# Kernel optimization log

Hardware: AMD Instinct MI355X
Metric: run time of the kernel (lower is better)

## Reference

```python
import jax, jax.numpy as jnp
import numpy as np

B, N, D, DH = 8, 2048, 1024, 64

def setup_inputs() -> dict:
    key = jax.random.key(0)
    ks = jax.random.split(key, 4)
    s = 1.0 / np.sqrt(D)
    return {
        "x": jax.random.normal(ks[0], (B, N, D), dtype=jnp.float32),
        "Wq": jax.random.normal(ks[1], (D, DH), dtype=jnp.float32) * s,
        "bq": jnp.zeros((DH,), dtype=jnp.float32),
        "Wk": jax.random.normal(ks[2], (D, DH), dtype=jnp.float32) * s,
        "bk": jnp.zeros((DH,), dtype=jnp.float32),
        "Wv": jax.random.normal(ks[3], (D, DH), dtype=jnp.float32) * s,
        "bv": jnp.zeros((DH,), dtype=jnp.float32),
    }

def reference(x, Wq, bq, Wk, bk, Wv, bv):
    # Projections: [B,N,DH]
    Q = x @ Wq + bq
    K = x @ Wk + bk
    V = x @ Wv + bv
    sqrt_dh = jnp.sqrt(jnp.asarray(DH, dtype=x.dtype))
    # scores[b,i,j] = Q_i . K_j  (original materializes [B,N,N,DH]; GEMM is equivalent math)
    att = jnp.einsum("bid,bjd->bij", Q, K) / sqrt_dh
    # NOTE: original softmaxes over dim=1 (the query/i axis), not the usual j axis.
    att = jax.nn.softmax(att, axis=1)
    # Dropout is identity in eval mode.
    return jnp.einsum("bij,bjd->bid", att, V)
```

## Files before the change

### kernel.cpp

```cpp
#include <hip/hip_runtime.h>
#include <math.h>

#define Bn  8
#define Nn  2048
#define Dn  1024
#define DHn 64
#define PAD  72
#define PADP 72

typedef __attribute__((ext_vector_type(8))) short bf16x8;
typedef __attribute__((ext_vector_type(4))) float f32x4;

static __device__ inline short f2bf(float f) {
    unsigned u = __builtin_bit_cast(unsigned, f);
    u += 0x7FFFu + ((u >> 16) & 1u);
    return (short)(u >> 16);
}
static __device__ inline bf16x8 pack8(float4 a, float4 b) {
    bf16x8 v;
    v[0] = f2bf(a.x); v[1] = f2bf(a.y); v[2] = f2bf(a.z); v[3] = f2bf(a.w);
    v[4] = f2bf(b.x); v[5] = f2bf(b.y); v[6] = f2bf(b.z); v[7] = f2bf(b.w);
    return v;
}

__global__ __launch_bounds__(128) void wt_kernel(
    const float* __restrict__ Wq, const float* __restrict__ Wk,
    const float* __restrict__ Wv, short* __restrict__ Wtf)
{
    const int nt = blockIdx.x / 16, kt = blockIdx.x % 16;
    const int t = threadIdx.x;
    const int half = t >> 6, l = t & 63;
    const int c = l & 15, quad = l >> 4;
    const int mat = nt >> 2, cm = (nt & 3) * 16 + c;
    const float* Wm = (mat == 0) ? Wq : (mat == 1 ? Wk : Wv);
    short* o = &Wtf[((((size_t)nt * 16 + kt) * 2 + half) * 64 + l) * 8];
#pragma unroll
    for (int e = 0; e < 8; ++e) {
        const int k = kt * 64 + half * 32 + quad * 8 + e;
        o[e] = f2bf(Wm[(size_t)k * DHn + cm]);
    }
}

__global__ __launch_bounds__(256) void qkv_kernel(
    const float* __restrict__ x, const short* __restrict__ Wtf,
    const float* __restrict__ bq, const float* __restrict__ bk,
    const float* __restrict__ bv,
    short* __restrict__ Qb, short* __restrict__ Kb, short* __restrict__ Vt)
{
    __shared__ __attribute__((aligned(16))) short xs[2][32][PAD];

    const int t = threadIdx.x;
    const int w = t >> 6, l = t & 63;
    const int c = l & 15, quad = l >> 4;
    const int ibase = blockIdx.x * 32;
    const int r0 = t >> 3, kc = t & 7;

    const float* xrow = &x[(size_t)(ibase + r0) * Dn + kc * 8];

    {
        const float4 a = ((const float4*)xrow)[0];
        const float4 b = ((const float4*)xrow)[1];
        *(bf16x8*)&xs[0][r0][kc * 8] = pack8(a, b);
    }

    f32x4 acc[2][3];
#pragma unroll
    for (int mt = 0; mt < 2; ++mt)
#pragma unroll
        for (int nt = 0; nt < 3; ++nt) acc[mt][nt] = (f32x4){0.f, 0.f, 0.f, 0.f};

    __syncthreads();

    for (int kt = 0; kt < 16; ++kt) {
        const int cur = kt & 1;
        float4 pa, pb;
        if (kt < 15) {
            pa = ((const float4*)(xrow + (kt + 1) * 64))[0];
            pb = ((const float4*)(xrow + (kt + 1) * 64))[1];
        }
#pragma unroll
        for (int h = 0; h < 2; ++h) {
            const bf16x8 af0 = *(const bf16x8*)&xs[cur][c][h * 32 + quad * 8];
            const bf16x8 af1 = *(const bf16x8*)&xs[cur][16 + c][h * 32 + quad * 8];
#pragma unroll
            for (int nt = 0; nt < 3; ++nt) {
                const int ntg = w * 3 + nt;
                const bf16x8 bf = *(const bf16x8*)&Wtf[((((size_t)ntg * 16 + kt) * 2 + h) * 64 + l) * 8];
                acc[0][nt] = __builtin_amdgcn_mfma_f32_16x16x32_bf16(af0, bf, acc[0][nt], 0, 0, 0);
                acc[1][nt] = __builtin_amdgcn_mfma_f32_16x16x32_bf16(af1, bf, acc[1][nt], 0, 0, 0);
            }
        }
        if (kt < 15) *(bf16x8*)&xs[1 - cur][r0][kc * 8] = pack8(pa, pb);
        __syncthreads();
    }

#pragma unroll
    for (int nt = 0; nt < 3; ++nt) {
        const int col = w * 48 + nt * 16 + c;
        const int mat = col >> 6, cm = col & 63;
        const float bias = (mat == 0 ? bq : (mat == 1 ? bk : bv))[cm];
#pragma unroll
        for (int mt = 0; mt < 2; ++mt) {
            if (mat == 2) {
                const int row = ibase + mt * 16 + quad * 4;
                const int b = row >> 11, i = row & (Nn - 1);
                ushort4 o;
                o.x = (unsigned short)f2bf(acc[mt][nt][0] + bias);
                o.y = (unsigned short)f2bf(acc[mt][nt][1] + bias);
                o.z = (unsigned short)f2bf(acc[mt][nt][2] + bias);
                o.w = (unsigned short)f2bf(acc[mt][nt][3] + bias);
                *(ushort4*)&Vt[((size_t)b * DHn + cm) * Nn + i] = o;
            } else {
                const float s = (mat == 1) ? 0.125f : 1.0f;
                short* Out = (mat == 0) ? Qb : Kb;
#pragma unroll
                for (int r = 0; r < 4; ++r)
                    Out[(size_t)(ibase + mt * 16 + quad * 4 + r) * DHn + cm] =
                        f2bf((acc[mt][nt][r] + bias) * s);
            }
        }
    }
}

__global__ __launch_bounds__(256) void colsum_kernel(
    const short* __restrict__ Qb, const short* __restrict__ Kb,
    float* __restrict__ lpart)
{
    __shared__ __attribute__((aligned(16))) short Qw[4][2][32][PAD];
    __shared__ float red[16][64];

    const int t = threadIdx.x;
    const int w = t >> 6, l = t & 63;
    const int c = l & 15, quad = l >> 4;
    const int bid = blockIdx.x;
    const int b = bid >> 7, rem = bid & 127, jt = rem >> 2, s = rem & 3;
    const int jbase = jt * 64;
    const int srow = l >> 1, scoff = (l & 1) * 32;

    bf16x8 kb[4][2];
#pragma unroll
    for (int nt = 0; nt < 4; ++nt)
#pragma unroll
        for (int kk = 0; kk < 2; ++kk)
            kb[nt][kk] = *(const bf16x8*)&Kb[((size_t)b * Nn + jbase + nt * 16 + c) * DHn
                                             + kk * 32 + quad * 8];

    const short* qbase = &Qb[((size_t)b * Nn + s * 512 + w * 128 + srow) * DHn + scoff];

#pragma unroll
    for (int k = 0; k < 4; ++k)
        *(bf16x8*)&Qw[w][0][srow][scoff + k * 8] = *(const bf16x8*)(qbase + k * 8);

    float lsum[4] = {0.f, 0.f, 0.f, 0.f};

    for (int it2 = 0; it2 < 4; ++it2) {
        const int cur = it2 & 1;
        bf16x8 p[4];
        if (it2 < 3) {
            const short* pq = qbase + (size_t)(it2 + 1) * 32 * DHn;
#pragma unroll
            for (int k = 0; k < 4; ++k) p[k] = *(const bf16x8*)(pq + k * 8);
        }
#pragma unroll
        for (int cc2 = 0; cc2 < 2; ++cc2) {
            const bf16x8 aq0 = *(const bf16x8*)&Qw[w][cur][cc2 * 16 + c][quad * 8];
            const bf16x8 aq1 = *(const bf16x8*)&Qw[w][cur][cc2 * 16 + c][32 + quad * 8];
#pragma unroll
            for (int nt = 0; nt < 4; ++nt) {
                f32x4 sv = (f32x4){0.f, 0.f, 0.f, 0.f};
                sv = __builtin_amdgcn_mfma_f32_16x16x32_bf16(aq0, kb[nt][0], sv, 0, 0, 0);
                sv = __builtin_amdgcn_mfma_f32_16x16x32_bf16(aq1, kb[nt][1], sv, 0, 0, 0);
                lsum[nt] += __expf(sv[0]) + __expf(sv[1]) + __expf(sv[2]) + __expf(sv[3]);
            }
        }
        if (it2 < 3) {
#pragma unroll
            for (int k = 0; k < 4; ++k)
                *(bf16x8*)&Qw[w][1 - cur][srow][scoff + k * 8] = p[k];
        }
    }

#pragma unroll
    for (int nt = 0; nt < 4; ++nt) red[w * 4 + quad][nt * 16 + c] = lsum[nt];
    __syncthreads();
    if (t < 64) {
        float sum = 0.f;
#pragma unroll
        for (int r = 0; r < 16; ++r) sum += red[r][t];
        lpart[((size_t)s * Bn + b) * Nn + jbase + t] = sum;
    }
}

__global__ __launch_bounds__(256) void attnout_kernel(
    const short* __restrict__ Qb, const short* __restrict__ Kb,
    const short* __restrict__ Vt, const float* __restrict__ lpart,
    float* __restrict__ outp)
{
    __shared__ __attribute__((aligned(16))) short Ks[2][64][PAD];
    __shared__ __attribute__((aligned(16))) short Vs[2][64][PAD];
    __shared__ __attribute__((aligned(16))) short Ps[4][32][PADP];
    __shared__ float rls[2][64];

    const int t = threadIdx.x;
    const int w = t >> 6, lane = t & 63;
    const int c = lane & 15, quad = lane >> 4;
    const int bid = blockIdx.x;
    const int b = bid >> 7, rem = bid & 127, it = rem >> 3, s = rem & 7;
    const int ibase = it * 128;
    const int r0 = t >> 2, cc = (t & 3) * 16;

    bf16x8 aq[2][2];
#pragma unroll
    for (int sub = 0; sub < 2; ++sub) {
        const size_t qrow = (size_t)b * Nn + ibase + w * 32 + sub * 16 + c;
        aq[sub][0] = *(const bf16x8*)&Qb[qrow * DHn + quad * 8];
        aq[sub][1] = *(const bf16x8*)&Qb[qrow * DHn + 32 + quad * 8];
    }

    const short* kbase = &Kb[((size_t)b * Nn + s * 256 + r0) * DHn + cc];
    const short* vbase = &Vt[((size_t)b * DHn + r0) * Nn + s * 256 + cc];

    *(bf16x8*)&Ks[0][r0][cc]     = *(const bf16x8*)kbase;
    *(bf16x8*)&Ks[0][r0][cc + 8] = *(const bf16x8*)(kbase + 8);
    *(bf16x8*)&Vs[0][r0][cc]     = *(const bf16x8*)vbase;
    *(bf16x8*)&Vs[0][r0][cc + 8] = *(const bf16x8*)(vbase + 8);
    if (t < 64) {
        const size_t lj = (size_t)b * Nn + s * 256 + t;
        rls[0][t] = 1.0f / (lpart[lj] + lpart[(size_t)Bn * Nn + lj]
                          + lpart[2 * (size_t)Bn * Nn + lj] + lpart[3 * (size_t)Bn * Nn + lj]);
    }

    f32x4 acc[2][4];
#pragma unroll
    for (int sub = 0; sub < 2; ++sub)
#pragma unroll
        for (int dn = 0; dn < 4; ++dn) acc[sub][dn] = (f32x4){0.f, 0.f, 0.f, 0.f};
    __syncthreads();

    for (int jt2 = 0; jt2 < 4; ++jt2) {
        const int cur = jt2 & 1;
        bf16x8 pk0, pk1, pv0, pv1; float nrl;
        if (jt2 < 3) {
            const short* pk = kbase + (size_t)(jt2 + 1) * 64 * DHn;
            pk0 = *(const bf16x8*)pk; pk1 = *(const bf16x8*)(pk + 8);
            const short* pv = vbase + (jt2 + 1) * 64;
            pv0 = *(const bf16x8*)pv; pv1 = *(const bf16x8*)(pv + 8);
            if (t < 64) {
                const size_t lj = (size_t)b * Nn + s * 256 + (jt2 + 1) * 64 + t;
                nrl = 1.0f / (lpart[lj] + lpart[(size_t)Bn * Nn + lj]
                            + lpart[2 * (size_t)Bn * Nn + lj] + lpart[3 * (size_t)Bn * Nn + lj]);
            }
        }

#pragma unroll
        for (int nt = 0; nt < 4; ++nt) {
            const bf16x8 kb0 = *(const bf16x8*)&Ks[cur][nt * 16 + c][quad * 8];
            const bf16x8 kb1 = *(const bf16x8*)&Ks[cur][nt * 16 + c][32 + quad * 8];
            const float rl = rls[cur][nt * 16 + c];
#pragma unroll
            for (int sub = 0; sub < 2; ++sub) {
                f32x4 sv = (f32x4){0.f, 0.f, 0.f, 0.f};
                sv = __builtin_amdgcn_mfma_f32_16x16x32_bf16(aq[sub][0], kb0, sv, 0, 0, 0);
                sv = __builtin_amdgcn_mfma_f32_16x16x32_bf16(aq[sub][1], kb1, sv, 0, 0, 0);
#pragma unroll
                for (int r = 0; r < 4; ++r)
                    Ps[w][sub * 16 + quad * 4 + r][nt * 16 + c] = f2bf(__expf(sv[r]) * rl);
            }
        }
        bf16x8 ap[2][2];
#pragma unroll
        for (int sub = 0; sub < 2; ++sub) {
            ap[sub][0] = *(const bf16x8*)&Ps[w][sub * 16 + c][quad * 8];
            ap[sub][1] = *(const bf16x8*)&Ps[w][sub * 16 + c][32 + quad * 8];
        }
#pragma unroll
        for (int dn = 0; dn < 4; ++dn) {
            const bf16x8 vb0 = *(const bf16x8*)&Vs[cur][dn * 16 + c][quad * 8];
            const bf16x8 vb1 = *(const bf16x8*)&Vs[cur][dn * 16 + c][32 + quad * 8];
#pragma unroll
            for (int sub = 0; sub < 2; ++sub) {
                acc[sub][dn] = __builtin_amdgcn_mfma_f32_16x16x32_bf16(ap[sub][0], vb0, acc[sub][dn], 0, 0, 0);
                acc[sub][dn] = __builtin_amdgcn_mfma_f32_16x16x32_bf16(ap[sub][1], vb1, acc[sub][dn], 0, 0, 0);
            }
        }

        if (jt2 < 3) {
            *(bf16x8*)&Ks[1 - cur][r0][cc]     = pk0;
            *(bf16x8*)&Ks[1 - cur][r0][cc + 8] = pk1;
            *(bf16x8*)&Vs[1 - cur][r0][cc]     = pv0;
            *(bf16x8*)&Vs[1 - cur][r0][cc + 8] = pv1;
            if (t < 64) rls[1 - cur][t] = nrl;
        }
        __syncthreads();
    }

    float* op = outp + (size_t)s * (Bn * Nn * DHn) + ((size_t)b * Nn + ibase) * DHn;
#pragma unroll
    for (int sub = 0; sub < 2; ++sub)
#pragma unroll
        for (int dn = 0; dn < 4; ++dn)
#pragma unroll
            for (int r = 0; r < 4; ++r)
                op[(w * 32 + sub * 16 + quad * 4 + r) * DHn + dn * 16 + c] = acc[sub][dn][r];
}

__global__ __launch_bounds__(256) void outreduce_kernel(
    const float* __restrict__ outp, float* __restrict__ out)
{
    const int id = blockIdx.x * 256 + threadIdx.x;
    const float4* p = (const float4*)outp;
    float4 r = p[id];
#pragma unroll
    for (int k = 1; k < 8; ++k) {
        const float4 a = p[id + (size_t)k * 262144];
        r.x += a.x; r.y += a.y; r.z += a.z; r.w += a.w;
    }
    ((float4*)out)[id] = r;
}

extern "C" void kernel_launch(void* const* d_in, const int* in_sizes, int n_in,
                              void* d_out, int out_size, void* d_ws, size_t ws_size,
                              hipStream_t stream)
{
    const float* x  = (const float*)d_in[0];
    const float* Wq = (const float*)d_in[1];
    const float* bq = (const float*)d_in[2];
    const float* Wk = (const float*)d_in[3];
    const float* bk = (const float*)d_in[4];
    const float* Wv = (const float*)d_in[5];
    const float* bv = (const float*)d_in[6];
    float* out = (float*)d_out;

    char* ws = (char*)d_ws;
    short* Qb    = (short*)(ws);
    short* Kb    = (short*)(ws + (size_t)(1 << 21));
    short* Vt    = (short*)(ws + (size_t)(2 << 21));
    short* Wtf   = (short*)(ws + (size_t)(3 << 21));
    float* lpart = (float*)(ws + (size_t)(3 << 21) + (1 << 19));
    float* outp  = (float*)(ws + (size_t)(7 << 20));

    wt_kernel<<<dim3(192), dim3(128), 0, stream>>>(Wq, Wk, Wv, Wtf);
    qkv_kernel<<<dim3(512), dim3(256), 0, stream>>>(x, Wtf, bq, bk, bv, Qb, Kb, Vt);
    colsum_kernel<<<dim3(1024), dim3(256), 0, stream>>>(Qb, Kb, lpart);
    attnout_kernel<<<dim3(1024), dim3(256), 0, stream>>>(Qb, Kb, Vt, lpart, outp);
    outreduce_kernel<<<dim3(1024), dim3(256), 0, stream>>>(outp, out);
}
```

Measured before the change: 156.4 us.

## Fold column-softmax normalization into V and halve attnout key splits

The qkv kernel now writes V in fp32. A new vscale kernel divides V by the column sums and converts it to bf16, which removes the per-key reciprocal loads and multiplies from attnout. attnout handles 512 keys per block across 512 blocks, writes P transposed through swapped MFMA operands, and outreduce sums 4 partials instead of 8. Block index mapping is reordered so that batch is the fastest-varying dimension. The cost is an extra kernel launch, an fp32 V round trip through memory, and fewer attnout blocks, which lowers parallelism.

Measured after the change: 151.7 us. -3.0%, faster.

```diff
diff --git a/kernel.cpp b/kernel.cpp
--- a/kernel.cpp
+++ b/kernel.cpp
@@ -45,7 +45,7 @@
     const float* __restrict__ x, const short* __restrict__ Wtf,
     const float* __restrict__ bq, const float* __restrict__ bk,
     const float* __restrict__ bv,
-    short* __restrict__ Qb, short* __restrict__ Kb, short* __restrict__ Vt)
+    short* __restrict__ Qb, short* __restrict__ Kb, float* __restrict__ Vtf32)
 {
     __shared__ __attribute__((aligned(16))) short xs[2][32][PAD];
 
@@ -104,12 +104,12 @@
             if (mat == 2) {
                 const int row = ibase + mt * 16 + quad * 4;
                 const int b = row >> 11, i = row & (Nn - 1);
-                ushort4 o;
-                o.x = (unsigned short)f2bf(acc[mt][nt][0] + bias);
-                o.y = (unsigned short)f2bf(acc[mt][nt][1] + bias);
-                o.z = (unsigned short)f2bf(acc[mt][nt][2] + bias);
-                o.w = (unsigned short)f2bf(acc[mt][nt][3] + bias);
-                *(ushort4*)&Vt[((size_t)b * DHn + cm) * Nn + i] = o;
+                float4 o;
+                o.x = acc[mt][nt][0] + bias;
+                o.y = acc[mt][nt][1] + bias;
+                o.z = acc[mt][nt][2] + bias;
+                o.w = acc[mt][nt][3] + bias;
+                *(float4*)&Vtf32[((size_t)b * DHn + cm) * Nn + i] = o;
             } else {
                 const float s = (mat == 1) ? 0.125f : 1.0f;
                 short* Out = (mat == 0) ? Qb : Kb;
@@ -133,7 +133,7 @@
     const int w = t >> 6, l = t & 63;
     const int c = l & 15, quad = l >> 4;
     const int bid = blockIdx.x;
-    const int b = bid >> 7, rem = bid & 127, jt = rem >> 2, s = rem & 3;
+    const int b = bid & 7, jt = (bid >> 3) & 31, s = (bid >> 8) & 3;
     const int jbase = jt * 64;
     const int srow = l >> 1, scoff = (l & 1) * 32;
 
@@ -191,21 +191,47 @@
     }
 }
 
+__global__ __launch_bounds__(256) void vscale_kernel(
+    const float* __restrict__ lpart, const float* __restrict__ Vtf32,
+    short* __restrict__ Vt)
+{
+    const int idx = blockIdx.x * 256 + threadIdx.x;
+    const int b = idx >> 14;
+    const int d = (idx >> 8) & 63;
+    const int j0 = (idx & 255) * 8;
+    const size_t off = ((size_t)b * DHn + d) * Nn + j0;
+    const size_t lj = (size_t)b * Nn + j0;
+
+    const float* l0 = &lpart[lj];
+    float4 sa = ((const float4*)l0)[0];
+    float4 sb = ((const float4*)l0)[1];
+#pragma unroll
+    for (int s = 1; s < 4; ++s) {
+        const float4 a = ((const float4*)(l0 + (size_t)s * Bn * Nn))[0];
+        const float4 c = ((const float4*)(l0 + (size_t)s * Bn * Nn))[1];
+        sa.x += a.x; sa.y += a.y; sa.z += a.z; sa.w += a.w;
+        sb.x += c.x; sb.y += c.y; sb.z += c.z; sb.w += c.w;
+    }
+    float4 va = ((const float4*)&Vtf32[off])[0];
+    float4 vb = ((const float4*)&Vtf32[off])[1];
+    va.x /= sa.x; va.y /= sa.y; va.z /= sa.z; va.w /= sa.w;
+    vb.x /= sb.x; vb.y /= sb.y; vb.z /= sb.z; vb.w /= sb.w;
+    *(bf16x8*)&Vt[off] = pack8(va, vb);
+}
+
 __global__ __launch_bounds__(256) void attnout_kernel(
     const short* __restrict__ Qb, const short* __restrict__ Kb,
-    const short* __restrict__ Vt, const float* __restrict__ lpart,
-    float* __restrict__ outp)
+    const short* __restrict__ Vt, float* __restrict__ outp)
 {
     __shared__ __attribute__((aligned(16))) short Ks[2][64][PAD];
     __shared__ __attribute__((aligned(16))) short Vs[2][64][PAD];
-    __shared__ __attribute__((aligned(16))) short Ps[4][32][PADP];
-    __shared__ float rls[2][64];
+    __shared__ __attribute__((aligned(16))) short Pt[4][2][16][PADP];
 
     const int t = threadIdx.x;
     const int w = t >> 6, lane = t & 63;
     const int c = lane & 15, quad = lane >> 4;
     const int bid = blockIdx.x;
-    const int b = bid >> 7, rem = bid & 127, it = rem >> 3, s = rem & 7;
+    const int b = bid & 7, rem = bid >> 3, it = rem >> 2, s = rem & 3;
     const int ibase = it * 128;
     const int r0 = t >> 2, cc = (t & 3) * 16;
 
@@ -217,18 +243,13 @@
         aq[sub][1] = *(const bf16x8*)&Qb[qrow * DHn + 32 + quad * 8];
     }
 
-    const short* kbase = &Kb[((size_t)b * Nn + s * 256 + r0) * DHn + cc];
-    const short* vbase = &Vt[((size_t)b * DHn + r0) * Nn + s * 256 + cc];
+    const short* kbase = &Kb[((size_t)b * Nn + s * 512 + r0) * DHn + cc];
+    const short* vbase = &Vt[((size_t)b * DHn + r0) * Nn + s * 512 + cc];
 
     *(bf16x8*)&Ks[0][r0][cc]     = *(const bf16x8*)kbase;
     *(bf16x8*)&Ks[0][r0][cc + 8] = *(const bf16x8*)(kbase + 8);
     *(bf16x8*)&Vs[0][r0][cc]     = *(const bf16x8*)vbase;
     *(bf16x8*)&Vs[0][r0][cc + 8] = *(const bf16x8*)(vbase + 8);
-    if (t < 64) {
-        const size_t lj = (size_t)b * Nn + s * 256 + t;
-        rls[0][t] = 1.0f / (lpart[lj] + lpart[(size_t)Bn * Nn + lj]
-                          + lpart[2 * (size_t)Bn * Nn + lj] + lpart[3 * (size_t)Bn * Nn + lj]);
-    }
 
     f32x4 acc[2][4];
 #pragma unroll
@@ -237,41 +258,38 @@
         for (int dn = 0; dn < 4; ++dn) acc[sub][dn] = (f32x4){0.f, 0.f, 0.f, 0.f};
     __syncthreads();
 
-    for (int jt2 = 0; jt2 < 4; ++jt2) {
+    for (int jt2 = 0; jt2 < 8; ++jt2) {
         const int cur = jt2 & 1;
-        bf16x8 pk0, pk1, pv0, pv1; float nrl;
-        if (jt2 < 3) {
+        bf16x8 pk0, pk1, pv0, pv1;
+        if (jt2 < 7) {
             const short* pk = kbase + (size_t)(jt2 + 1) * 64 * DHn;
             pk0 = *(const bf16x8*)pk; pk1 = *(const bf16x8*)(pk + 8);
             const short* pv = vbase + (jt2 + 1) * 64;
             pv0 = *(const bf16x8*)pv; pv1 = *(const bf16x8*)(pv + 8);
-            if (t < 64) {
-                const size_t lj = (size_t)b * Nn + s * 256 + (jt2 + 1) * 64 + t;
-                nrl = 1.0f / (lpart[lj] + lpart[(size_t)Bn * Nn + lj]
-                            + lpart[2 * (size_t)Bn * Nn + lj] + lpart[3 * (size_t)Bn * Nn + lj]);
-            }
         }
 
 #pragma unroll
         for (int nt = 0; nt < 4; ++nt) {
             const bf16x8 kb0 = *(const bf16x8*)&Ks[cur][nt * 16 + c][quad * 8];
             const bf16x8 kb1 = *(const bf16x8*)&Ks[cur][nt * 16 + c][32 + quad * 8];
-            const float rl = rls[cur][nt * 16 + c];
 #pragma unroll
             for (int sub = 0; sub < 2; ++sub) {
                 f32x4 sv = (f32x4){0.f, 0.f, 0.f, 0.f};
-                sv = __builtin_amdgcn_mfma_f32_16x16x32_bf16(aq[sub][0], kb0, sv, 0, 0, 0);
-                sv = __builtin_amdgcn_mfma_f32_16x16x32_bf16(aq[sub][1], kb1, sv, 0, 0, 0);
-#pragma unroll
-                for (int r = 0; r < 4; ++r)
-                    Ps[w][sub * 16 + quad * 4 + r][nt * 16 + c] = f2bf(__expf(sv[r]) * rl);
+                sv = __builtin_amdgcn_mfma_f32_16x16x32_bf16(kb0, aq[sub][0], sv, 0, 0, 0);
+                sv = __builtin_amdgcn_mfma_f32_16x16x32_bf16(kb1, aq[sub][1], sv, 0, 0, 0);
+                ushort4 o;
+                o.x = (unsigned short)f2bf(__expf(sv[0]));
+                o.y = (unsigned short)f2bf(__expf(sv[1]));
+                o.z = (unsigned short)f2bf(__expf(sv[2]));
+                o.w = (unsigned short)f2bf(__expf(sv[3]));
+                *(ushort4*)&Pt[w][sub][c][nt * 16 + quad * 4] = o;
             }
         }
         bf16x8 ap[2][2];
 #pragma unroll
         for (int sub = 0; sub < 2; ++sub) {
-            ap[sub][0] = *(const bf16x8*)&Ps[w][sub * 16 + c][quad * 8];
-            ap[sub][1] = *(const bf16x8*)&Ps[w][sub * 16 + c][32 + quad * 8];
+            ap[sub][0] = *(const bf16x8*)&Pt[w][sub][c][quad * 8];
+            ap[sub][1] = *(const bf16x8*)&Pt[w][sub][c][32 + quad * 8];
         }
 #pragma unroll
         for (int dn = 0; dn < 4; ++dn) {
@@ -284,12 +302,11 @@
             }
         }
 
-        if (jt2 < 3) {
+        if (jt2 < 7) {
             *(bf16x8*)&Ks[1 - cur][r0][cc]     = pk0;
             *(bf16x8*)&Ks[1 - cur][r0][cc + 8] = pk1;
             *(bf16x8*)&Vs[1 - cur][r0][cc]     = pv0;
             *(bf16x8*)&Vs[1 - cur][r0][cc + 8] = pv1;
-            if (t < 64) rls[1 - cur][t] = nrl;
         }
         __syncthreads();
     }
@@ -311,7 +328,7 @@
     const float4* p = (const float4*)outp;
     float4 r = p[id];
 #pragma unroll
-    for (int k = 1; k < 8; ++k) {
+    for (int k = 1; k < 4; ++k) {
         const float4 a = p[id + (size_t)k * 262144];
         r.x += a.x; r.y += a.y; r.z += a.z; r.w += a.w;
     }
@@ -337,11 +354,13 @@
     short* Vt    = (short*)(ws + (size_t)(2 << 21));
     short* Wtf   = (short*)(ws + (size_t)(3 << 21));
     float* lpart = (float*)(ws + (size_t)(3 << 21) + (1 << 19));
-    float* outp  = (float*)(ws + (size_t)(7 << 20));
+    float* Vtf32 = (float*)(ws + (size_t)(7 << 20));
+    float* outp  = (float*)(ws + (size_t)(11 << 20));
 
     wt_kernel<<<dim3(192), dim3(128), 0, stream>>>(Wq, Wk, Wv, Wtf);
-    qkv_kernel<<<dim3(512), dim3(256), 0, stream>>>(x, Wtf, bq, bk, bv, Qb, Kb, Vt);
+    qkv_kernel<<<dim3(512), dim3(256), 0, stream>>>(x, Wtf, bq, bk, bv, Qb, Kb, Vtf32);
     colsum_kernel<<<dim3(1024), dim3(256), 0, stream>>>(Qb, Kb, lpart);
-    attnout_kernel<<<dim3(1024), dim3(256), 0, stream>>>(Qb, Kb, Vt, lpart, outp);
+    vscale_kernel<<<dim3(512), dim3(256), 0, stream>>>(lpart, Vtf32, Vt);
+    attnout_kernel<<<dim3(512), dim3(256), 0, stream>>>(Qb, Kb, Vt, outp);
     outreduce_kernel<<<dim3(1024), dim3(256), 0, stream>>>(outp, out);
 }
```
